# Performance work log

Hardware: AMD Instinct MI355X
Metric: run time of the kernel (lower is better)

Reference implementation:

```python
import jax, jax.numpy as jnp
import numpy as np

N, E, B = 65536, 262144, 2048   # nodes, edges, graphs
ND, ED, H, L = 32, 8, 128, 4    # node feat, edge feat, hidden, egnn layers
PE, PH, CH = 1280, 512, 512     # protein embed, protein hidden, combined hidden
EPS = 1e-8


def _seg_mean(data, ids, num):
    s = jax.ops.segment_sum(data, ids, num_segments=num)
    c = jax.ops.segment_sum(jnp.ones((data.shape[0], 1), data.dtype), ids, num_segments=num)
    return s / jnp.clip(c, 1.0)


def setup_inputs() -> dict:
    key = jax.random.key(0)
    ks = iter(jax.random.split(key, 40))

    def p(shape, scale=0.05):
        return jax.random.normal(next(ks), shape, dtype=jnp.float32) * scale

    inp = {
        "x": jax.random.normal(next(ks), (N, ND), dtype=jnp.float32),
        "pos": jax.random.normal(next(ks), (N, 3), dtype=jnp.float32),
        "edge_attr": jax.random.uniform(next(ks), (E, ED), dtype=jnp.float32),
        "protein_embedding": jax.random.normal(next(ks), (B, PE), dtype=jnp.float32),
        "edge_index": jax.random.randint(next(ks), (2, E), 0, N),
        "batch": jnp.arange(N, dtype=jnp.int64) // (N // B),
        # EGNN embeddings
        "emb_in_w": p((ND, H)), "emb_in_b": p((H,)),
        "emb_out_w": p((H, H)), "emb_out_b": p((H,)),
        # per-layer stacked params (leading dim L)
        "edge_w1": p((L, 2 * H + 1 + ED, H)), "edge_b1": p((L, H)),
        "edge_w2": p((L, H, H)), "edge_b2": p((L, H)),
        "att_w": p((L, H, 1)), "att_b": p((L, 1)),
        "coord_w1": p((L, H, H)), "coord_b1": p((L, H)),
        "coord_w2": p((L, H, 1)),  # no bias, xavier in torch impl
        "node_w1": p((L, 2 * H, H)), "node_b1": p((L, H)),
        "node_w2": p((L, H, H)), "node_b2": p((L, H)),
        # protein + combined heads
        "prot_w": p((PE, PH)), "prot_b": p((PH,)),
        "comb_w1": p((H + PH, CH)), "comb_b1": p((CH,)),
        "comb_w2": p((CH, 1)), "comb_b2": p((1,)),
    }
    return inp


def _forward(x, pos, edge_attr, protein_embedding,
             emb_in_w, emb_in_b, emb_out_w, emb_out_b,
             edge_w1, edge_b1, edge_w2, edge_b2, att_w, att_b,
             coord_w1, coord_b1, coord_w2,
             node_w1, node_b1, node_w2, node_b2,
             prot_w, prot_b, comb_w1, comb_b1, comb_w2, comb_b2,
             edge_index, batch):
    row, col = edge_index[0], edge_index[1]
    h = x @ emb_in_w + emb_in_b
    for l in range(L):
        # coord2radial (normalize=True)
        d = pos[row] - pos[col]                       # [E,3]
        radial = jnp.sum(d * d, axis=-1, keepdims=True)  # [E,1]
        d = d / (jnp.sqrt(radial) + EPS)
        # edge model with sigmoid attention gate
        e_in = jnp.concatenate([h[row], h[col], radial, edge_attr], axis=-1)
        m = jax.nn.silu(e_in @ edge_w1[l] + edge_b1[l])
        m = jax.nn.silu(m @ edge_w2[l] + edge_b2[l])
        m = m * jax.nn.sigmoid(m @ att_w[l] + att_b[l])
        # coord model (tanh=True, coords_agg='mean')
        t = jax.nn.silu(m @ coord_w1[l] + coord_b1[l])
        trans = d * jnp.tanh(t @ coord_w2[l])         # [E,3]
        pos = pos + _seg_mean(trans, row, N)
        # node model (sum aggregation, residual)
        agg = jax.ops.segment_sum(m, row, num_segments=N)
        nh = jax.nn.silu(jnp.concatenate([h, agg], axis=-1) @ node_w1[l] + node_b1[l])
        h = h + (nh @ node_w2[l] + node_b2[l])
    h = h @ emb_out_w + emb_out_b
    # global mean pool over graphs
    drug = _seg_mean(h, batch, B)                     # [B,H]
    prot = jax.nn.relu(protein_embedding @ prot_w + prot_b)  # dropout = identity (eval)
    c = jnp.concatenate([drug, prot], axis=-1)
    c = jax.nn.relu(c @ comb_w1 + comb_b1)
    logits = (c @ comb_w2 + comb_b2)[:, 0]
    return logits


def reference(x, pos, edge_attr, protein_embedding,
              emb_in_w, emb_in_b, emb_out_w, emb_out_b,
              edge_w1, edge_b1, edge_w2, edge_b2, att_w, att_b,
              coord_w1, coord_b1, coord_w2,
              node_w1, node_b1, node_w2, node_b2,
              prot_w, prot_b, comb_w1, comb_b1, comb_w2, comb_b2,
              edge_index, batch):
    logits = _forward(x, pos, edge_attr, protein_embedding,
                      emb_in_w, emb_in_b, emb_out_w, emb_out_b,
                      edge_w1, edge_b1, edge_w2, edge_b2, att_w, att_b,
                      coord_w1, coord_b1, coord_w2,
                      node_w1, node_b1, node_w2, node_b2,
                      prot_w, prot_b, comb_w1, comb_b1, comb_w2, comb_b2,
                      edge_index, batch)
    attention_weights = jnp.zeros((B, 1, 1), dtype=logits.dtype)
    return logits, attention_weights
```

## Files before the change

### kernel.cpp

```cpp
#include <hip/hip_runtime.h>
#include <math.h>


static constexpr int NN  = 65536;
static constexpr int NE  = 262144;
static constexpr int NB  = 2048;
static constexpr int NDF = 32;
static constexpr int HD  = 128;
static constexpr int NL  = 4;
static constexpr int PED = 1280;
static constexpr int PHD = 512;
static constexpr int CHD = 512;
static constexpr float EPSV = 1e-8f;

static constexpr int KK1 = 9;
static constexpr int KK2 = 4;
static constexpr int KKN1 = 8;
static constexpr int KKP = 40;
static constexpr int KKC = 20;

static constexpr int ES = 36;

typedef __attribute__((ext_vector_type(8))) short bf8_t;
typedef __attribute__((ext_vector_type(4))) float f4_t;

__device__ __forceinline__ float sigmoid_f(float x) {
  return __fdividef(1.0f, 1.0f + __expf(-x));
}
__device__ __forceinline__ float silu_f(float x) { return x * sigmoid_f(x); }

__device__ __forceinline__ ushort f2bf(float f) {
  unsigned u = __float_as_uint(f);
  u += 0x7FFFu + ((u >> 16) & 1u);
  return (ushort)(u >> 16);
}
__device__ __forceinline__ float bf2f(ushort h) {
  return __uint_as_float(((unsigned)h) << 16);
}

__device__ __forceinline__ void fma44(float (&acc)[4][4], const float4 a, const float4 w) {
  const float av[4] = {a.x, a.y, a.z, a.w};
  const float wv[4] = {w.x, w.y, w.z, w.w};
#pragma unroll
  for (int i = 0; i < 4; ++i)
#pragma unroll
    for (int j = 0; j < 4; ++j) acc[i][j] = fmaf(av[i], wv[j], acc[i][j]);
}


__global__ void hist_kernel(const int* __restrict__ ei, int* __restrict__ deg) {
  const int e = blockIdx.x * 256 + threadIdx.x;
  if (e < NE) atomicAdd(&deg[ei[e]], 1);
}
// ... 24 lines not shown
    }
    __syncthreads();
    row_ptr[i + 1] = wsums[wave] + incl;
    __syncthreads();
  }
}

__global__ void fill_kernel(const int* __restrict__ ei, const int* __restrict__ row_ptr,
                            int* __restrict__ fill_pos, int* __restrict__ edge_ids) {
  const int e = blockIdx.x * 256 + threadIdx.x;
  if (e < NE) {
    const int n = ei[e];
    const int s = atomicAdd(&fill_pos[n], 1);
    edge_ids[row_ptr[n] + s] = e;
  }
}

__global__ void pos_copy_kernel(const float* __restrict__ pos, float* __restrict__ pc) {
  const int n = blockIdx.x * 256 + threadIdx.x;
  if (n < NN) {
    const float4 v = make_float4(pos[(size_t)n * 3 + 0], pos[(size_t)n * 3 + 1],
                                 pos[(size_t)n * 3 + 2], 0.0f);
    *(float4*)(pc + (size_t)n * 4) = v;
  }
}


__global__ __launch_bounds__(256) void packw_kernel(
    const float* __restrict__ W, ushort* __restrict__ Wp,
    int K, int N, int KK, size_t sW, size_t sWp) {
// ... 13 lines not shown
  for (int p = 0; p < 4; ++p) {
    const int ka = k0 + p * 2, kb = ka + 1;
    const unsigned lo = (ka < K) ? f2bf(w[(size_t)ka * N + n]) : 0;
    const unsigned hi = (kb < K) ? f2bf(w[(size_t)kb * N + n]) : 0;
    ww[p] = lo | (hi << 16);
  }
  *(uint4*)(Wp + layer * sWp + (size_t)i * 8) = make_uint4(ww[0], ww[1], ww[2], ww[3]);
}

__global__ __launch_bounds__(256) void cvt_bf_kernel(const float* __restrict__ in,
                                                     ushort* __restrict__ out, int n) {
  const int i = blockIdx.x * 256 + threadIdx.x;
  if (i * 8 >= n) return;
  const float4 v0 = *(const float4*)(in + (size_t)i * 8);
  const float4 v1 = *(const float4*)(in + (size_t)i * 8 + 4);
  unsigned w0 = (unsigned)f2bf(v0.x) | ((unsigned)f2bf(v0.y) << 16);
  unsigned w1 = (unsigned)f2bf(v0.z) | ((unsigned)f2bf(v0.w) << 16);
  unsigned w2 = (unsigned)f2bf(v1.x) | ((unsigned)f2bf(v1.y) << 16);
  unsigned w3 = (unsigned)f2bf(v1.z) | ((unsigned)f2bf(v1.w) << 16);
  *(uint4*)(out + (size_t)i * 8) = make_uint4(w0, w1, w2, w3);
}


__global__ __launch_bounds__(256) void geom_kernel(
    const float* __restrict__ pos_cur, const float* __restrict__ edge_attr,
    const int* __restrict__ ei, float* __restrict__ dnb, ushort* __restrict__ extra) {
  const int e = blockIdx.x * 256 + threadIdx.x;
  if (e >= NE) return;
  const int r = ei[e], c = ei[NE + e];
  const float4 pr = *(const float4*)(pos_cur + (size_t)r * 4);
  const float4 pc = *(const float4*)(pos_cur + (size_t)c * 4);
  const float dx = pr.x - pc.x, dy = pr.y - pc.y, dz = pr.z - pc.z;
  const float radial = dx * dx + dy * dy + dz * dz;
  const float inv = 1.0f / (sqrtf(radial) + EPSV);
  *(float4*)(dnb + (size_t)e * 4) = make_float4(dx * inv, dy * inv, dz * inv, 0.0f);
  const float4 ea0 = *(const float4*)(edge_attr + (size_t)e * 8);
  const float4 ea1 = *(const float4*)(edge_attr + (size_t)e * 8 + 4);
  const unsigned w0 = (unsigned)f2bf(radial) | ((unsigned)f2bf(ea0.x) << 16);
  const unsigned w1 = (unsigned)f2bf(ea0.y) | ((unsigned)f2bf(ea0.z) << 16);
  const unsigned w2 = (unsigned)f2bf(ea0.w) | ((unsigned)f2bf(ea1.x) << 16);
  const unsigned w3 = (unsigned)f2bf(ea1.y) | ((unsigned)f2bf(ea1.z) << 16);
  const unsigned w4 = (unsigned)f2bf(ea1.w);
  ushort* dst = extra + (size_t)e * 32;
  *(uint4*)(dst)      = make_uint4(w0, w1, w2, w3);
  *(uint4*)(dst + 8)  = make_uint4(w4, 0, 0, 0);
  *(uint4*)(dst + 16) = make_uint4(0, 0, 0, 0);
  *(uint4*)(dst + 24) = make_uint4(0, 0, 0, 0);
}


__global__ __launch_bounds__(256) void emb_in_kernel(
    const float* __restrict__ x, const float* __restrict__ W,
    const float* __restrict__ B, float* __restrict__ h, ushort* __restrict__ hbf) {
  __shared__ float xs[NDF * ES];
  const int t = threadIdx.x;
  const int n0 = blockIdx.x * 32;
  {
    const int r = t >> 3;
    const int kq = (t & 7) * 4;
    const float4 v = *(const float4*)(x + (size_t)(n0 + r) * NDF + kq);
// ... 7 lines not shown
  float acc[4][4] = {};
  const float* wp = W + fg * 4;
#pragma unroll
  for (int k = 0; k < NDF; ++k) {
    const float4 a = *(const float4*)&xs[k * ES + eg * 4];
    const float4 w = *(const float4*)(wp + (size_t)k * HD);
    fma44(acc, a, w);
  }
  const float4 bv = *(const float4*)(B + fg * 4);
  const float bb[4] = {bv.x, bv.y, bv.z, bv.w};
#pragma unroll
  for (int i = 0; i < 4; ++i) {
    const float4 o = make_float4(acc[i][0] + bb[0], acc[i][1] + bb[1],
                                 acc[i][2] + bb[2], acc[i][3] + bb[3]);
    *(float4*)(h + (size_t)(n0 + eg * 4 + i) * HD + fg * 4) = o;
    ushort4 hb;
    hb.x = f2bf(o.x); hb.y = f2bf(o.y); hb.z = f2bf(o.z); hb.w = f2bf(o.w);
    *(ushort4*)(hbf + (size_t)(n0 + eg * 4 + i) * HD + fg * 4) = hb;
  }
}


__global__ __launch_bounds__(256) void edge_mfma_kernel(
    const ushort* __restrict__ hbf, const ushort* __restrict__ extra,
    const int* __restrict__ edge_index, const float* __restrict__ dnb,
    const ushort* __restrict__ W1p, const float* __restrict__ B1,
    const ushort* __restrict__ W2p, const float* __restrict__ B2,
    const float* __restrict__ AW, const float* __restrict__ AB,
    const ushort* __restrict__ CW1p, const float* __restrict__ CB1,
    const float* __restrict__ CW2,
    ushort* __restrict__ m_bf, float* __restrict__ trans_out) {
  __shared__ ushort mtile[64 * 128];
  __shared__ int ridx[64], cidx[64];
  __shared__ float redbuf[2][64];
  __shared__ float gates[64];

  const int t = threadIdx.x;
  const int e0 = blockIdx.x * 64;
  if (t < 64) {
    ridx[t] = edge_index[e0 + t];
    cidx[t] = edge_index[NE + e0 + t];
  }
  __syncthreads();

  const int w = t >> 6, l = t & 63;
  const int wr = w >> 1, wc = w & 1;
  const int g = l >> 4, ln = l & 15;
  const int row0 = wr * 32;

  int er[2], ec[2], rowA[2];
#pragma unroll
  for (int mt = 0; mt < 2; ++mt) {
    rowA[mt] = row0 + mt * 16 + ln;
    er[mt] = ridx[rowA[mt]];
    ec[mt] = cidx[rowA[mt]];
  }

  const f4_t zf = {0.0f, 0.0f, 0.0f, 0.0f};
  f4_t acc[2][4];
#pragma unroll
  for (int mt = 0; mt < 2; ++mt)
#pragma unroll
    for (int nt = 0; nt < 4; ++nt) acc[mt][nt] = zf;

#pragma unroll
  for (int kk = 0; kk < KK1; ++kk) {
    bf8_t a[2], b[4];
#pragma unroll
    for (int mt = 0; mt < 2; ++mt) {
      if (kk < 8) {
        const int idx = (kk < 4) ? er[mt] : ec[mt];
        a[mt] = *(const bf8_t*)(hbf + (size_t)idx * HD + (kk & 3) * 32 + g * 8);
      } else {
        a[mt] = *(const bf8_t*)(extra + (size_t)(e0 + rowA[mt]) * 32 + g * 8);
      }
    }
#pragma unroll
    for (int nt = 0; nt < 4; ++nt)
      b[nt] = *(const bf8_t*)(W1p + ((size_t)(kk * 8 + wc * 4 + nt) * 64 + l) * 8);
#pragma unroll
    for (int mt = 0; mt < 2; ++mt)
#pragma unroll
      for (int nt = 0; nt < 4; ++nt)
        acc[mt][nt] = __builtin_amdgcn_mfma_f32_16x16x32_bf16(a[mt], b[nt], acc[mt][nt], 0, 0, 0);
  }

  {
    float bn[4];
#pragma unroll
    for (int nt = 0; nt < 4; ++nt) bn[nt] = B1[wc * 64 + nt * 16 + ln];
#pragma unroll
    for (int mt = 0; mt < 2; ++mt)
#pragma unroll
      for (int nt = 0; nt < 4; ++nt) {
        const int col = wc * 64 + nt * 16 + ln;
#pragma unroll
        for (int r = 0; r < 4; ++r) {
          const int row = row0 + mt * 16 + g * 4 + r;
          const float v = silu_f(acc[mt][nt][r] + bn[nt]);
          mtile[row * HD + (col ^ ((row & 7) << 3))] = f2bf(v);
        }
      }
  }
  __syncthreads();

  f4_t acc2[2][4];
#pragma unroll
  for (int mt = 0; mt < 2; ++mt)
#pragma unroll
    for (int nt = 0; nt < 4; ++nt) acc2[mt][nt] = zf;
#pragma unroll
  for (int kk = 0; kk < KK2; ++kk) {
    bf8_t a[2], b[4];
#pragma unroll
    for (int mt = 0; mt < 2; ++mt) {
      const int ra = rowA[mt];
      const int k0 = kk * 32 + g * 8;
      a[mt] = *(const bf8_t*)&mtile[ra * HD + (k0 ^ ((ra & 7) << 3))];
    }
#pragma unroll
    for (int nt = 0; nt < 4; ++nt)
      b[nt] = *(const bf8_t*)(W2p + ((size_t)(kk * 8 + wc * 4 + nt) * 64 + l) * 8);
#pragma unroll
    for (int mt = 0; mt < 2; ++mt)
#pragma unroll
      for (int nt = 0; nt < 4; ++nt)
        acc2[mt][nt] = __builtin_amdgcn_mfma_f32_16x16x32_bf16(a[mt], b[nt], acc2[mt][nt], 0, 0, 0);
  }

  float m2v[2][4][4];
  {
    float bn[4], awv[4];
#pragma unroll
    for (int nt = 0; nt < 4; ++nt) {
      const int col = wc * 64 + nt * 16 + ln;
      bn[nt] = B2[col];
      awv[nt] = AW[col];
    }
    float p[2][4] = {{0, 0, 0, 0}, {0, 0, 0, 0}};
#pragma unroll
    for (int mt = 0; mt < 2; ++mt)
#pragma unroll
      for (int nt = 0; nt < 4; ++nt)
#pragma unroll
        for (int r = 0; r < 4; ++r) {
          const float v = silu_f(acc2[mt][nt][r] + bn[nt]);
          m2v[mt][nt][r] = v;
          p[mt][r] = fmaf(v, awv[nt], p[mt][r]);
        }
#pragma unroll
    for (int mt = 0; mt < 2; ++mt)
#pragma unroll
      for (int r = 0; r < 4; ++r) {
#pragma unroll
        for (int d = 1; d < 16; d <<= 1) p[mt][r] += __shfl_xor(p[mt][r], d, 64);
      }
    if (ln == 0) {
#pragma unroll
      for (int mt = 0; mt < 2; ++mt)
#pragma unroll
        for (int r = 0; r < 4; ++r)
          redbuf[wc][row0 + mt * 16 + g * 4 + r] = p[mt][r];
    }
  }
  __syncthreads();
  if (t < 64) gates[t] = sigmoid_f(redbuf[0][t] + redbuf[1][t] + AB[0]);
  __syncthreads();

  {
    float grow[2][4];
#pragma unroll
    for (int mt = 0; mt < 2; ++mt)
#pragma unroll
      for (int r = 0; r < 4; ++r) grow[mt][r] = gates[row0 + mt * 16 + g * 4 + r];
#pragma unroll
    for (int mt = 0; mt < 2; ++mt)
#pragma unroll
      for (int nt = 0; nt < 4; ++nt) {
        const int col = wc * 64 + nt * 16 + ln;
#pragma unroll
        for (int r = 0; r < 4; ++r) {
          const int row = row0 + mt * 16 + g * 4 + r;
          mtile[row * HD + (col ^ ((row & 7) << 3))] = f2bf(m2v[mt][nt][r] * grow[mt][r]);
        }
      }
  }
  __syncthreads();

  f4_t acc3[2][4];
#pragma unroll
  for (int mt = 0; mt < 2; ++mt)
#pragma unroll
    for (int nt = 0; nt < 4; ++nt) acc3[mt][nt] = zf;
#pragma unroll
  for (int kk = 0; kk < KK2; ++kk) {
    bf8_t a[2], b[4];
#pragma unroll
    for (int mt = 0; mt < 2; ++mt) {
      const int ra = rowA[mt];
      const int k0 = kk * 32 + g * 8;
      a[mt] = *(const bf8_t*)&mtile[ra * HD + (k0 ^ ((ra & 7) << 3))];
    }
#pragma unroll
    for (int nt = 0; nt < 4; ++nt)
      b[nt] = *(const bf8_t*)(CW1p + ((size_t)(kk * 8 + wc * 4 + nt) * 64 + l) * 8);
#pragma unroll
    for (int mt = 0; mt < 2; ++mt)
#pragma unroll
      for (int nt = 0; nt < 4; ++nt)
        acc3[mt][nt] = __builtin_amdgcn_mfma_f32_16x16x32_bf16(a[mt], b[nt], acc3[mt][nt], 0, 0, 0);
  }
  {
    float cb[4], cwv[4];
#pragma unroll
    for (int nt = 0; nt < 4; ++nt) {
      const int col = wc * 64 + nt * 16 + ln;
      cb[nt] = CB1[col];
      cwv[nt] = CW2[col];
    }
    float q[2][4] = {{0, 0, 0, 0}, {0, 0, 0, 0}};
#pragma unroll
    for (int mt = 0; mt < 2; ++mt)
#pragma unroll
      for (int nt = 0; nt < 4; ++nt)
#pragma unroll
        for (int r = 0; r < 4; ++r) {
          const float v = silu_f(acc3[mt][nt][r] + cb[nt]);
          q[mt][r] = fmaf(v, cwv[nt], q[mt][r]);
        }
#pragma unroll
    for (int mt = 0; mt < 2; ++mt)
#pragma unroll
      for (int r = 0; r < 4; ++r) {
#pragma unroll
        for (int d = 1; d < 16; d <<= 1) q[mt][r] += __shfl_xor(q[mt][r], d, 64);
      }
    if (ln == 0) {
#pragma unroll
      for (int mt = 0; mt < 2; ++mt)
#pragma unroll
        for (int r = 0; r < 4; ++r)
          redbuf[wc][row0 + mt * 16 + g * 4 + r] = q[mt][r];
    }
  }
  __syncthreads();
  if (t < 64) {
    const float s = tanhf(redbuf[0][t] + redbuf[1][t]);
    const f4_t dn = *(const f4_t*)(dnb + (size_t)(e0 + t) * 4);
    const f4_t tr = dn * s;
    *(f4_t*)(trans_out + (size_t)(e0 + t) * 4) = tr;
  }

#pragma unroll
  for (int it = 0; it < 4; ++it) {
    const int i = it * 256 + t;
    const int row = i >> 4;
    const int c8 = (i & 15) * 8;
    const uint4 v = *(const uint4*)&mtile[row * HD + (c8 ^ ((row & 7) << 3))];
    *(uint4*)(m_bf + (size_t)(e0 + row) * HD + c8) = v;
  }
}


__global__ __launch_bounds__(256) void gather_kernel(
    const ushort* __restrict__ m_bf, const float* __restrict__ trans,
    const int* __restrict__ row_ptr, const int* __restrict__ edge_ids,
    ushort* __restrict__ agg_bf, float* __restrict__ pos_cur) {
  const int t = threadIdx.x;
  const int wave = t >> 6, lane = t & 63;
  const int n = blockIdx.x * 4 + wave;
  const int s = row_ptr[n], e_end = row_ptr[n + 1];
  float a0 = 0.0f, a1 = 0.0f, ta = 0.0f;
  for (int i = s; i < e_end; ++i) {
    const int e = edge_ids[i];
    const ushort2 v = *(const ushort2*)(m_bf + (size_t)e * HD + lane * 2);
    a0 += bf2f(v.x);
    a1 += bf2f(v.y);
    if (lane < 4) ta += trans[(size_t)e * 4 + lane];
  }
  ushort2 ab;
  ab.x = f2bf(a0);
  ab.y = f2bf(a1);
  *(ushort2*)(agg_bf + (size_t)n * HD + lane * 2) = ab;
  if (lane < 3) {
    const int dg = e_end - s;
    pos_cur[(size_t)n * 4 + lane] += ta / (float)(dg > 0 ? dg : 1);
  }
}


__global__ __launch_bounds__(256) void node_mfma_kernel(
    float* __restrict__ h, const ushort* __restrict__ hbf,
    const ushort* __restrict__ agg_bf,
    const ushort* __restrict__ W1p, const float* __restrict__ B1,
    const ushort* __restrict__ W2p, const float* __restrict__ B2,
    ushort* __restrict__ hbf_out) {
  __shared__ ushort mtile[64 * 128];
  const int t = threadIdx.x;
  const int n0 = blockIdx.x * 64;
  const int w = t >> 6, l = t & 63;
  const int wr = w >> 1, wc = w & 1;
  const int g = l >> 4, ln = l & 15;
  const int row0 = wr * 32;
  int rowA[2];
#pragma unroll
  for (int mt = 0; mt < 2; ++mt) rowA[mt] = row0 + mt * 16 + ln;

  const f4_t zf = {0.0f, 0.0f, 0.0f, 0.0f};
  f4_t acc[2][4];
#pragma unroll
  for (int mt = 0; mt < 2; ++mt)
#pragma unroll
    for (int nt = 0; nt < 4; ++nt) acc[mt][nt] = zf;

#pragma unroll
  for (int kk = 0; kk < KKN1; ++kk) {
    bf8_t a[2], b[4];
#pragma unroll
    for (int mt = 0; mt < 2; ++mt) {
      const size_t base = (size_t)(n0 + rowA[mt]) * HD + (kk & 3) * 32 + g * 8;
      a[mt] = (kk < 4) ? *(const bf8_t*)(hbf + base) : *(const bf8_t*)(agg_bf + base);
    }
#pragma unroll
    for (int nt = 0; nt < 4; ++nt)
      b[nt] = *(const bf8_t*)(W1p + ((size_t)(kk * 8 + wc * 4 + nt) * 64 + l) * 8);
#pragma unroll
    for (int mt = 0; mt < 2; ++mt)
#pragma unroll
      for (int nt = 0; nt < 4; ++nt)
        acc[mt][nt] = __builtin_amdgcn_mfma_f32_16x16x32_bf16(a[mt], b[nt], acc[mt][nt], 0, 0, 0);
  }
  {
    float bn[4];
#pragma unroll
    for (int nt = 0; nt < 4; ++nt) bn[nt] = B1[wc * 64 + nt * 16 + ln];
#pragma unroll
    for (int mt = 0; mt < 2; ++mt)
#pragma unroll
      for (int nt = 0; nt < 4; ++nt) {
        const int col = wc * 64 + nt * 16 + ln;
#pragma unroll
        for (int r = 0; r < 4; ++r) {
          const int row = row0 + mt * 16 + g * 4 + r;
          const float v = silu_f(acc[mt][nt][r] + bn[nt]);
          mtile[row * HD + (col ^ ((row & 7) << 3))] = f2bf(v);
        }
      }
  }
  __syncthreads();

  f4_t acc2[2][4];
#pragma unroll
  for (int mt = 0; mt < 2; ++mt)
#pragma unroll
    for (int nt = 0; nt < 4; ++nt) acc2[mt][nt] = zf;
#pragma unroll
  for (int kk = 0; kk < KK2; ++kk) {
    bf8_t a[2], b[4];
#pragma unroll
    for (int mt = 0; mt < 2; ++mt) {
      const int ra = rowA[mt];
      const int k0 = kk * 32 + g * 8;
      a[mt] = *(const bf8_t*)&mtile[ra * HD + (k0 ^ ((ra & 7) << 3))];
    }
#pragma unroll
    for (int nt = 0; nt < 4; ++nt)
      b[nt] = *(const bf8_t*)(W2p + ((size_t)(kk * 8 + wc * 4 + nt) * 64 + l) * 8);
#pragma unroll
    for (int mt = 0; mt < 2; ++mt)
#pragma unroll
      for (int nt = 0; nt < 4; ++nt)
        acc2[mt][nt] = __builtin_amdgcn_mfma_f32_16x16x32_bf16(a[mt], b[nt], acc2[mt][nt], 0, 0, 0);
  }
  {
    float bn[4];
#pragma unroll
    for (int nt = 0; nt < 4; ++nt) bn[nt] = B2[wc * 64 + nt * 16 + ln];
#pragma unroll
    for (int mt = 0; mt < 2; ++mt)
#pragma unroll
      for (int nt = 0; nt < 4; ++nt) {
        const int col = wc * 64 + nt * 16 + ln;
#pragma unroll
        for (int r = 0; r < 4; ++r) {
          const int row = row0 + mt * 16 + g * 4 + r;
          float* hp = h + (size_t)(n0 + row) * HD + col;
          const float o = *hp + acc2[mt][nt][r] + bn[nt];
          *hp = o;
          hbf_out[(size_t)(n0 + row) * HD + col] = f2bf(o);
        }
      }
  }
}


__global__ __launch_bounds__(256) void gemm_head_kernel(
    const ushort* __restrict__ A, const ushort* __restrict__ Wp,
    const float* __restrict__ bias, ushort* __restrict__ out,
    int lda, int KK, int NTG, int ldo, int col_off) {
  const int t = threadIdx.x;
  const int rb = blockIdx.x * 64;
  const int cb = blockIdx.y * 128;
  const int w = t >> 6, l = t & 63;
  const int wr = w >> 1, wc = w & 1;
  const int g = l >> 4, ln = l & 15;
  const int row0 = wr * 32;
// ... 115 lines not shown

  char* ws = (char*)d_ws;
  size_t off = 0;
  auto carve = [&](size_t bytes) -> void* {
    void* p = ws + off;
    off += (bytes + 255) & ~(size_t)255;
    return p;
  };
  float*  h       = (float*)carve((size_t)NN * HD * 4);
  ushort* h_bf    = (ushort*)carve((size_t)NN * HD * 2);
  ushort* agg_bf  = (ushort*)carve((size_t)NN * HD * 2);
  ushort* m_bf    = (ushort*)carve((size_t)NE * HD * 2);
  float*  trans   = (float*)carve((size_t)NE * 4 * 4);
  float*  dnb     = (float*)carve((size_t)NE * 4 * 4);
  ushort* extra   = (ushort*)carve((size_t)NE * 32 * 2);
  float*  pos_cur = (float*)carve((size_t)NN * 4 * 4);
  ushort* pe_bf   = (ushort*)carve((size_t)NB * PED * 2);
  ushort* c_in    = (ushort*)carve((size_t)NB * (HD + PHD) * 2);
  ushort* c1      = (ushort*)carve((size_t)NB * CHD * 2);
  const size_t sW1p  = (size_t)KK1 * 8 * 64 * 8;
  const size_t sW2p  = (size_t)KK2 * 8 * 64 * 8;
  const size_t sNW1p = (size_t)KKN1 * 8 * 64 * 8;
  const size_t sPWp  = (size_t)KKP * 32 * 64 * 8;
  const size_t sCWp  = (size_t)KKC * 32 * 64 * 8;
  ushort* W1p     = (ushort*)carve(sW1p * NL * 2);
  ushort* W2p     = (ushort*)carve(sW2p * NL * 2);
  ushort* CW1p    = (ushort*)carve(sW2p * NL * 2);
  ushort* NW1p    = (ushort*)carve(sNW1p * NL * 2);
  ushort* NW2p    = (ushort*)carve(sW2p * NL * 2);
  ushort* PWp     = (ushort*)carve(sPWp * 2);
  ushort* CWp     = (ushort*)carve(sCWp * 2);
  int* deg        = (int*)carve((size_t)NN * 4);
  int* row_ptr    = (int*)carve((size_t)(NN + 1) * 4);
  int* fill_pos   = (int*)carve((size_t)NN * 4);
  int* edge_ids   = (int*)carve((size_t)NE * 4);

  hipMemsetAsync(deg, 0, (size_t)NN * 4, stream);
  hipMemsetAsync(fill_pos, 0, (size_t)NN * 4, stream);

  pos_copy_kernel<<<NN / 256, 256, 0, stream>>>(pos, pos_cur);
  hist_kernel<<<NE / 256, 256, 0, stream>>>(edge_index, deg);
  scan_kernel<<<1, 1024, 0, stream>>>(deg, row_ptr);
  fill_kernel<<<NE / 256, 256, 0, stream>>>(edge_index, row_ptr, fill_pos, edge_ids);

  packw_kernel<<<dim3(18, NL), 256, 0, stream>>>(edge_w1, W1p, 265, HD, KK1,
                                                 (size_t)265 * HD, sW1p);
  packw_kernel<<<dim3(8, NL), 256, 0, stream>>>(edge_w2, W2p, HD, HD, KK2,
                                                (size_t)HD * HD, sW2p);
  packw_kernel<<<dim3(8, NL), 256, 0, stream>>>(coord_w1, CW1p, HD, HD, KK2,
                                                (size_t)HD * HD, sW2p);
  packw_kernel<<<dim3(16, NL), 256, 0, stream>>>(node_w1, NW1p, 2 * HD, HD, KKN1,
                                                 (size_t)2 * HD * HD, sNW1p);
  packw_kernel<<<dim3(8, NL), 256, 0, stream>>>(node_w2, NW2p, HD, HD, KK2,
                                                (size_t)HD * HD, sW2p);
  packw_kernel<<<dim3(320, 1), 256, 0, stream>>>(prot_w, PWp, PED, PHD, KKP, 0, 0);
  packw_kernel<<<dim3(160, 1), 256, 0, stream>>>(comb_w1, CWp, HD + PHD, CHD, KKC, 0, 0);

  cvt_bf_kernel<<<NB * PED / (256 * 8), 256, 0, stream>>>(pe, pe_bf, NB * PED);

  emb_in_kernel<<<NN / 32, 256, 0, stream>>>(x, emb_in_w, emb_in_b, h, h_bf);

  for (int l = 0; l < NL; ++l) {
    geom_kernel<<<NE / 256, 256, 0, stream>>>(pos_cur, edge_attr, edge_index,
                                              dnb, extra);
    edge_mfma_kernel<<<NE / 64, 256, 0, stream>>>(
        h_bf, extra, edge_index, dnb,
        W1p + (size_t)l * sW1p, edge_b1 + (size_t)l * HD,
        W2p + (size_t)l * sW2p, edge_b2 + (size_t)l * HD,
        att_w + (size_t)l * HD, att_b + l,
        CW1p + (size_t)l * sW2p, coord_b1 + (size_t)l * HD,
        coord_w2 + (size_t)l * HD,
        m_bf, trans);
    gather_kernel<<<NN / 4, 256, 0, stream>>>(m_bf, trans, row_ptr, edge_ids,
                                              agg_bf, pos_cur);
    node_mfma_kernel<<<NN / 64, 256, 0, stream>>>(
        h, h_bf, agg_bf,
        NW1p + (size_t)l * sNW1p, node_b1 + (size_t)l * HD,
        NW2p + (size_t)l * sW2p, node_b2 + (size_t)l * HD, h_bf);
  }

  pool_kernel<<<NB, 128, 0, stream>>>(h, emb_out_w, emb_out_b, c_in);
  gemm_head_kernel<<<dim3(NB / 64, PHD / 128), 256, 0, stream>>>(
      pe_bf, PWp, prot_b, c_in, PED, KKP, PHD / 16, HD + PHD, HD);
  gemm_head_kernel<<<dim3(NB / 64, CHD / 128), 256, 0, stream>>>(
      c_in, CWp, comb_b1, c1, HD + PHD, KKC, CHD / 16, CHD, 0);
  logits_kernel<<<NB / 4, 256, 0, stream>>>(c1, comb_w2, comb_b2, out);
}
```

Measured before the change: 1.094 ms.

## Sort edges by destination and transpose MFMA operand roles in edge/node kernels

Edges are permuted once into CSR order (row/col and edge_attr copied into sorted buffers), so the per-layer geometry and edge kernels produce messages already grouped by source node. The gather kernel can then read messages contiguously instead of going through an edge_ids indirection. The edge and node MFMA kernels also swap operand roles: weights become the A operand and edges or nodes the B operand. This gives each lane four contiguous output features, which allows vectorised bias loads, packed bf16 stores and shorter shuffle reductions. The cost is a one-time permutation pass plus extra buffers for the sorted indices and attributes.

```diff
diff --git a/kernel.cpp b/kernel.cpp
--- a/kernel.cpp
+++ b/kernel.cpp
@@ -37,6 +37,9 @@
 __device__ __forceinline__ float bf2f(ushort h) {
   return __uint_as_float(((unsigned)h) << 16);
 }
+__device__ __forceinline__ unsigned pk2bf(float a, float b) {
+  return (unsigned)f2bf(a) | ((unsigned)f2bf(b) << 16);
+}
 
 __device__ __forceinline__ void fma44(float (&acc)[4][4], const float4 a, const float4 w) {
   const float av[4] = {a.x, a.y, a.z, a.w};
@@ -91,6 +94,21 @@
     const int s = atomicAdd(&fill_pos[n], 1);
     edge_ids[row_ptr[n] + s] = e;
   }
+}
+
+__global__ void perm_kernel(const int* __restrict__ ei, const int* __restrict__ edge_ids,
+                            const float* __restrict__ edge_attr,
+                            int* __restrict__ rowp, int* __restrict__ colp,
+                            float* __restrict__ eap) {
+  const int i = blockIdx.x * 256 + threadIdx.x;
+  if (i >= NE) return;
+  const int e = edge_ids[i];
+  rowp[i] = ei[e];
+  colp[i] = ei[NE + e];
+  const float4 a = *(const float4*)(edge_attr + (size_t)e * 8);
+  const float4 b = *(const float4*)(edge_attr + (size_t)e * 8 + 4);
+  *(float4*)(eap + (size_t)i * 8) = a;
+  *(float4*)(eap + (size_t)i * 8 + 4) = b;
 }
 
 __global__ void pos_copy_kernel(const float* __restrict__ pos, float* __restrict__ pc) {
@@ -134,36 +152,30 @@
   if (i * 8 >= n) return;
   const float4 v0 = *(const float4*)(in + (size_t)i * 8);
   const float4 v1 = *(const float4*)(in + (size_t)i * 8 + 4);
-  unsigned w0 = (unsigned)f2bf(v0.x) | ((unsigned)f2bf(v0.y) << 16);
-  unsigned w1 = (unsigned)f2bf(v0.z) | ((unsigned)f2bf(v0.w) << 16);
-  unsigned w2 = (unsigned)f2bf(v1.x) | ((unsigned)f2bf(v1.y) << 16);
-  unsigned w3 = (unsigned)f2bf(v1.z) | ((unsigned)f2bf(v1.w) << 16);
-  *(uint4*)(out + (size_t)i * 8) = make_uint4(w0, w1, w2, w3);
+  *(uint4*)(out + (size_t)i * 8) =
+      make_uint4(pk2bf(v0.x, v0.y), pk2bf(v0.z, v0.w), pk2bf(v1.x, v1.y), pk2bf(v1.z, v1.w));
 }
 
 
 __global__ __launch_bounds__(256) void geom_kernel(
-    const float* __restrict__ pos_cur, const float* __restrict__ edge_attr,
-    const int* __restrict__ ei, float* __restrict__ dnb, ushort* __restrict__ extra) {
-  const int e = blockIdx.x * 256 + threadIdx.x;
-  if (e >= NE) return;
-  const int r = ei[e], c = ei[NE + e];
+    const float* __restrict__ pos_cur, const float* __restrict__ eap,
+    const int* __restrict__ rowp, const int* __restrict__ colp,
+    float* __restrict__ dnb, ushort* __restrict__ extra) {
+  const int i = blockIdx.x * 256 + threadIdx.x;
+  if (i >= NE) return;
+  const int r = rowp[i], c = colp[i];
   const float4 pr = *(const float4*)(pos_cur + (size_t)r * 4);
   const float4 pc = *(const float4*)(pos_cur + (size_t)c * 4);
   const float dx = pr.x - pc.x, dy = pr.y - pc.y, dz = pr.z - pc.z;
   const float radial = dx * dx + dy * dy + dz * dz;
   const float inv = 1.0f / (sqrtf(radial) + EPSV);
-  *(float4*)(dnb + (size_t)e * 4) = make_float4(dx * inv, dy * inv, dz * inv, 0.0f);
-  const float4 ea0 = *(const float4*)(edge_attr + (size_t)e * 8);
-  const float4 ea1 = *(const float4*)(edge_attr + (size_t)e * 8 + 4);
-  const unsigned w0 = (unsigned)f2bf(radial) | ((unsigned)f2bf(ea0.x) << 16);
-  const unsigned w1 = (unsigned)f2bf(ea0.y) | ((unsigned)f2bf(ea0.z) << 16);
-  const unsigned w2 = (unsigned)f2bf(ea0.w) | ((unsigned)f2bf(ea1.x) << 16);
-  const unsigned w3 = (unsigned)f2bf(ea1.y) | ((unsigned)f2bf(ea1.z) << 16);
-  const unsigned w4 = (unsigned)f2bf(ea1.w);
-  ushort* dst = extra + (size_t)e * 32;
-  *(uint4*)(dst)      = make_uint4(w0, w1, w2, w3);
-  *(uint4*)(dst + 8)  = make_uint4(w4, 0, 0, 0);
+  *(float4*)(dnb + (size_t)i * 4) = make_float4(dx * inv, dy * inv, dz * inv, 0.0f);
+  const float4 ea0 = *(const float4*)(eap + (size_t)i * 8);
+  const float4 ea1 = *(const float4*)(eap + (size_t)i * 8 + 4);
+  ushort* dst = extra + (size_t)i * 32;
+  *(uint4*)(dst) = make_uint4(pk2bf(radial, ea0.x), pk2bf(ea0.y, ea0.z),
+                              pk2bf(ea0.w, ea1.x), pk2bf(ea1.y, ea1.z));
+  *(uint4*)(dst + 8)  = make_uint4((unsigned)f2bf(ea1.w), 0, 0, 0);
   *(uint4*)(dst + 16) = make_uint4(0, 0, 0, 0);
   *(uint4*)(dst + 24) = make_uint4(0, 0, 0, 0);
 }
@@ -201,23 +213,23 @@
     const float4 o = make_float4(acc[i][0] + bb[0], acc[i][1] + bb[1],
                                  acc[i][2] + bb[2], acc[i][3] + bb[3]);
     *(float4*)(h + (size_t)(n0 + eg * 4 + i) * HD + fg * 4) = o;
-    ushort4 hb;
-    hb.x = f2bf(o.x); hb.y = f2bf(o.y); hb.z = f2bf(o.z); hb.w = f2bf(o.w);
-    *(ushort4*)(hbf + (size_t)(n0 + eg * 4 + i) * HD + fg * 4) = hb;
+    *(uint2*)(hbf + (size_t)(n0 + eg * 4 + i) * HD + fg * 4) =
+        make_uint2(pk2bf(o.x, o.y), pk2bf(o.z, o.w));
   }
 }
 
 
 __global__ __launch_bounds__(256) void edge_mfma_kernel(
     const ushort* __restrict__ hbf, const ushort* __restrict__ extra,
-    const int* __restrict__ edge_index, const float* __restrict__ dnb,
+    const int* __restrict__ rowp, const int* __restrict__ colp,
+    const float* __restrict__ dnb,
     const ushort* __restrict__ W1p, const float* __restrict__ B1,
     const ushort* __restrict__ W2p, const float* __restrict__ B2,
     const float* __restrict__ AW, const float* __restrict__ AB,
     const ushort* __restrict__ CW1p, const float* __restrict__ CB1,
     const float* __restrict__ CW2,
     ushort* __restrict__ m_bf, float* __restrict__ trans_out) {
-  __shared__ ushort mtile[64 * 128];
+  __shared__ ushort mtileT[64 * 128];
   __shared__ int ridx[64], cidx[64];
   __shared__ float redbuf[2][64];
   __shared__ float gates[64];
@@ -225,209 +237,186 @@
   const int t = threadIdx.x;
   const int e0 = blockIdx.x * 64;
   if (t < 64) {
-    ridx[t] = edge_index[e0 + t];
-    cidx[t] = edge_index[NE + e0 + t];
+    ridx[t] = rowp[e0 + t];
+    cidx[t] = colp[e0 + t];
   }
   __syncthreads();
 
   const int w = t >> 6, l = t & 63;
-  const int wr = w >> 1, wc = w & 1;
+  const int wn = w & 1, we = w >> 1;
   const int g = l >> 4, ln = l & 15;
-  const int row0 = wr * 32;
-
-  int er[2], ec[2], rowA[2];
-#pragma unroll
-  for (int mt = 0; mt < 2; ++mt) {
-    rowA[mt] = row0 + mt * 16 + ln;
-    er[mt] = ridx[rowA[mt]];
-    ec[mt] = cidx[rowA[mt]];
+  const int nb = wn * 64;
+  const int eb = we * 32;
+
+  int je[2], er[2], ec[2], swz[2];
+#pragma unroll
+  for (int et = 0; et < 2; ++et) {
+    je[et] = eb + et * 16 + ln;
+    er[et] = ridx[je[et]];
+    ec[et] = cidx[je[et]];
+    swz[et] = (je[et] & 7) << 3;
   }
 
   const f4_t zf = {0.0f, 0.0f, 0.0f, 0.0f};
-  f4_t acc[2][4];
-#pragma unroll
-  for (int mt = 0; mt < 2; ++mt)
-#pragma unroll
-    for (int nt = 0; nt < 4; ++nt) acc[mt][nt] = zf;
+  f4_t acc[4][2];
+#pragma unroll
+  for (int mt = 0; mt < 4; ++mt)
+#pragma unroll
+    for (int et = 0; et < 2; ++et) acc[mt][et] = zf;
 
 #pragma unroll
   for (int kk = 0; kk < KK1; ++kk) {
-    bf8_t a[2], b[4];
-#pragma unroll
-    for (int mt = 0; mt < 2; ++mt) {
+    bf8_t aw[4], be[2];
+#pragma unroll
+    for (int mt = 0; mt < 4; ++mt)
+      aw[mt] = *(const bf8_t*)(W1p + ((size_t)(kk * 8 + wn * 4 + mt) * 64 + l) * 8);
+#pragma unroll
+    for (int et = 0; et < 2; ++et) {
       if (kk < 8) {
-        const int idx = (kk < 4) ? er[mt] : ec[mt];
-        a[mt] = *(const bf8_t*)(hbf + (size_t)idx * HD + (kk & 3) * 32 + g * 8);
+        const int idx = (kk < 4) ? er[et] : ec[et];
+        be[et] = *(const bf8_t*)(hbf + (size_t)idx * HD + (kk & 3) * 32 + g * 8);
       } else {
-        a[mt] = *(const bf8_t*)(extra + (size_t)(e0 + rowA[mt]) * 32 + g * 8);
+        be[et] = *(const bf8_t*)(extra + (size_t)(e0 + je[et]) * 32 + g * 8);
       }
     }
 #pragma unroll
-    for (int nt = 0; nt < 4; ++nt)
-      b[nt] = *(const bf8_t*)(W1p + ((size_t)(kk * 8 + wc * 4 + nt) * 64 + l) * 8);
-#pragma unroll
-    for (int mt = 0; mt < 2; ++mt)
-#pragma unroll
-      for (int nt = 0; nt < 4; ++nt)
-        acc[mt][nt] = __builtin_amdgcn_mfma_f32_16x16x32_bf16(a[mt], b[nt], acc[mt][nt], 0, 0, 0);
+    for (int mt = 0; mt < 4; ++mt)
+#pragma unroll
+      for (int et = 0; et < 2; ++et)
+        acc[mt][et] = __builtin_amdgcn_mfma_f32_16x16x32_bf16(aw[mt], be[et], acc[mt][et], 0, 0, 0);
   }
 
   {
-    float bn[4];
-#pragma unroll
-    for (int nt = 0; nt < 4; ++nt) bn[nt] = B1[wc * 64 + nt * 16 + ln];
-#pragma unroll
-    for (int mt = 0; mt < 2; ++mt)
-#pragma unroll
-      for (int nt = 0; nt < 4; ++nt) {
-        const int col = wc * 64 + nt * 16 + ln;
+#pragma unroll
+    for (int mt = 0; mt < 4; ++mt) {
+      const int n0 = nb + mt * 16 + g * 4;
+      const float4 bv = *(const float4*)(B1 + n0);
+#pragma unroll
+      for (int et = 0; et < 2; ++et) {
+        const unsigned lo = pk2bf(silu_f(acc[mt][et][0] + bv.x), silu_f(acc[mt][et][1] + bv.y));
+        const unsigned hi = pk2bf(silu_f(acc[mt][et][2] + bv.z), silu_f(acc[mt][et][3] + bv.w));
+        *(uint2*)&mtileT[je[et] * HD + (n0 ^ swz[et])] = make_uint2(lo, hi);
+      }
+    }
+  }
+  __syncthreads();
+
+  f4_t acc2[4][2];
+#pragma unroll
+  for (int mt = 0; mt < 4; ++mt)
+#pragma unroll
+    for (int et = 0; et < 2; ++et) acc2[mt][et] = zf;
+#pragma unroll
+  for (int kk = 0; kk < KK2; ++kk) {
+    bf8_t aw[4], be[2];
+#pragma unroll
+    for (int mt = 0; mt < 4; ++mt)
+      aw[mt] = *(const bf8_t*)(W2p + ((size_t)(kk * 8 + wn * 4 + mt) * 64 + l) * 8);
+    const int nk = kk * 32 + g * 8;
+#pragma unroll
+    for (int et = 0; et < 2; ++et)
+      be[et] = *(const bf8_t*)&mtileT[je[et] * HD + (nk ^ swz[et])];
+#pragma unroll
+    for (int mt = 0; mt < 4; ++mt)
+#pragma unroll
+      for (int et = 0; et < 2; ++et)
+        acc2[mt][et] = __builtin_amdgcn_mfma_f32_16x16x32_bf16(aw[mt], be[et], acc2[mt][et], 0, 0, 0);
+  }
+
+  float m2v[4][2][4];
+  {
+    float p[2] = {0.0f, 0.0f};
+#pragma unroll
+    for (int mt = 0; mt < 4; ++mt) {
+      const int n0 = nb + mt * 16 + g * 4;
+      const float4 bv = *(const float4*)(B2 + n0);
+      const float4 av = *(const float4*)(AW + n0);
+      const float bb[4] = {bv.x, bv.y, bv.z, bv.w};
+      const float aa[4] = {av.x, av.y, av.z, av.w};
+#pragma unroll
+      for (int et = 0; et < 2; ++et)
 #pragma unroll
         for (int r = 0; r < 4; ++r) {
-          const int row = row0 + mt * 16 + g * 4 + r;
-          const float v = silu_f(acc[mt][nt][r] + bn[nt]);
-          mtile[row * HD + (col ^ ((row & 7) << 3))] = f2bf(v);
+          const float v = silu_f(acc2[mt][et][r] + bb[r]);
+          m2v[mt][et][r] = v;
+          p[et] = fmaf(v, aa[r], p[et]);
         }
+    }
+#pragma unroll
+    for (int et = 0; et < 2; ++et) {
+      p[et] += __shfl_xor(p[et], 16, 64);
+      p[et] += __shfl_xor(p[et], 32, 64);
+    }
+    if (l < 16) {
+#pragma unroll
+      for (int et = 0; et < 2; ++et) redbuf[wn][eb + et * 16 + l] = p[et];
+    }
+  }
+  __syncthreads();
+  if (t < 64) gates[t] = sigmoid_f(redbuf[0][t] + redbuf[1][t] + AB[0]);
+  __syncthreads();
+
+  {
+    float grow[2];
+#pragma unroll
+    for (int et = 0; et < 2; ++et) grow[et] = gates[je[et]];
+#pragma unroll
+    for (int mt = 0; mt < 4; ++mt) {
+      const int n0 = nb + mt * 16 + g * 4;
+#pragma unroll
+      for (int et = 0; et < 2; ++et) {
+        const unsigned lo = pk2bf(m2v[mt][et][0] * grow[et], m2v[mt][et][1] * grow[et]);
+        const unsigned hi = pk2bf(m2v[mt][et][2] * grow[et], m2v[mt][et][3] * grow[et]);
+        *(uint2*)&mtileT[je[et] * HD + (n0 ^ swz[et])] = make_uint2(lo, hi);
       }
-  }
-  __syncthreads();
-
-  f4_t acc2[2][4];
-#pragma unroll
-  for (int mt = 0; mt < 2; ++mt)
-#pragma unroll
-    for (int nt = 0; nt < 4; ++nt) acc2[mt][nt] = zf;
+    }
+  }
+  __syncthreads();
+
+  f4_t acc3[4][2];
+#pragma unroll
+  for (int mt = 0; mt < 4; ++mt)
+#pragma unroll
+    for (int et = 0; et < 2; ++et) acc3[mt][et] = zf;
 #pragma unroll
   for (int kk = 0; kk < KK2; ++kk) {
-    bf8_t a[2], b[4];
-#pragma unroll
-    for (int mt = 0; mt < 2; ++mt) {
-      const int ra = rowA[mt];
-      const int k0 = kk * 32 + g * 8;
-      a[mt] = *(const bf8_t*)&mtile[ra * HD + (k0 ^ ((ra & 7) << 3))];
-    }
-#pragma unroll
-    for (int nt = 0; nt < 4; ++nt)
-      b[nt] = *(const bf8_t*)(W2p + ((size_t)(kk * 8 + wc * 4 + nt) * 64 + l) * 8);
-#pragma unroll
-    for (int mt = 0; mt < 2; ++mt)
-#pragma unroll
-      for (int nt = 0; nt < 4; ++nt)
-        acc2[mt][nt] = __builtin_amdgcn_mfma_f32_16x16x32_bf16(a[mt], b[nt], acc2[mt][nt], 0, 0, 0);
-  }
-
-  float m2v[2][4][4];
+    bf8_t aw[4], be[2];
+#pragma unroll
+    for (int mt = 0; mt < 4; ++mt)
+      aw[mt] = *(const bf8_t*)(CW1p + ((size_t)(kk * 8 + wn * 4 + mt) * 64 + l) * 8);
+    const int nk = kk * 32 + g * 8;
+#pragma unroll
+    for (int et = 0; et < 2; ++et)
+      be[et] = *(const bf8_t*)&mtileT[je[et] * HD + (nk ^ swz[et])];
+#pragma unroll
+    for (int mt = 0; mt < 4; ++mt)
+#pragma unroll
+      for (int et = 0; et < 2; ++et)
+        acc3[mt][et] = __builtin_amdgcn_mfma_f32_16x16x32_bf16(aw[mt], be[et], acc3[mt][et], 0, 0, 0);
+  }
   {
-    float bn[4], awv[4];
-#pragma unroll
-    for (int nt = 0; nt < 4; ++nt) {
-      const int col = wc * 64 + nt * 16 + ln;
-      bn[nt] = B2[col];
-      awv[nt] = AW[col];
-    }
-    float p[2][4] = {{0, 0, 0, 0}, {0, 0, 0, 0}};
-#pragma unroll
-    for (int mt = 0; mt < 2; ++mt)
-#pragma unroll
-      for (int nt = 0; nt < 4; ++nt)
-#pragma unroll
-        for (int r = 0; r < 4; ++r) {
-          const float v = silu_f(acc2[mt][nt][r] + bn[nt]);
-          m2v[mt][nt][r] = v;
-          p[mt][r] = fmaf(v, awv[nt], p[mt][r]);
-        }
-#pragma unroll
-    for (int mt = 0; mt < 2; ++mt)
-#pragma unroll
-      for (int r = 0; r < 4; ++r) {
-#pragma unroll
-        for (int d = 1; d < 16; d <<= 1) p[mt][r] += __shfl_xor(p[mt][r], d, 64);
-      }
-    if (ln == 0) {
-#pragma unroll
-      for (int mt = 0; mt < 2; ++mt)
+    float q[2] = {0.0f, 0.0f};
+#pragma unroll
+    for (int mt = 0; mt < 4; ++mt) {
+      const int n0 = nb + mt * 16 + g * 4;
+      const float4 bv = *(const float4*)(CB1 + n0);
+      const float4 cv = *(const float4*)(CW2 + n0);
+      const float bb[4] = {bv.x, bv.y, bv.z, bv.w};
+      const float cc[4] = {cv.x, cv.y, cv.z, cv.w};
+#pragma unroll
+      for (int et = 0; et < 2; ++et)
 #pragma unroll
         for (int r = 0; r < 4; ++r)
-          redbuf[wc][row0 + mt * 16 + g * 4 + r] = p[mt][r];
-    }
-  }
-  __syncthreads();
-  if (t < 64) gates[t] = sigmoid_f(redbuf[0][t] + redbuf[1][t] + AB[0]);
-  __syncthreads();
-
-  {
-    float grow[2][4];
-#pragma unroll
-    for (int mt = 0; mt < 2; ++mt)
-#pragma unroll
-      for (int r = 0; r < 4; ++r) grow[mt][r] = gates[row0 + mt * 16 + g * 4 + r];
-#pragma unroll
-    for (int mt = 0; mt < 2; ++mt)
-#pragma unroll
-      for (int nt = 0; nt < 4; ++nt) {
-        const int col = wc * 64 + nt * 16 + ln;
-#pragma unroll
-        for (int r = 0; r < 4; ++r) {
-          const int row = row0 + mt * 16 + g * 4 + r;
-          mtile[row * HD + (col ^ ((row & 7) << 3))] = f2bf(m2v[mt][nt][r] * grow[mt][r]);
-        }
-      }
-  }
-  __syncthreads();
-
-  f4_t acc3[2][4];
-#pragma unroll
-  for (int mt = 0; mt < 2; ++mt)
-#pragma unroll
-    for (int nt = 0; nt < 4; ++nt) acc3[mt][nt] = zf;
-#pragma unroll
-  for (int kk = 0; kk < KK2; ++kk) {
-    bf8_t a[2], b[4];
-#pragma unroll
-    for (int mt = 0; mt < 2; ++mt) {
-      const int ra = rowA[mt];
-      const int k0 = kk * 32 + g * 8;
-      a[mt] = *(const bf8_t*)&mtile[ra * HD + (k0 ^ ((ra & 7) << 3))];
-    }
-#pragma unroll
-    for (int nt = 0; nt < 4; ++nt)
-      b[nt] = *(const bf8_t*)(CW1p + ((size_t)(kk * 8 + wc * 4 + nt) * 64 + l) * 8);
-#pragma unroll
-    for (int mt = 0; mt < 2; ++mt)
-#pragma unroll
-      for (int nt = 0; nt < 4; ++nt)
-        acc3[mt][nt] = __builtin_amdgcn_mfma_f32_16x16x32_bf16(a[mt], b[nt], acc3[mt][nt], 0, 0, 0);
-  }
-  {
-    float cb[4], cwv[4];
-#pragma unroll
-    for (int nt = 0; nt < 4; ++nt) {
-      const int col = wc * 64 + nt * 16 + ln;
-      cb[nt] = CB1[col];
-      cwv[nt] = CW2[col];
-    }
-    float q[2][4] = {{0, 0, 0, 0}, {0, 0, 0, 0}};
-#pragma unroll
-    for (int mt = 0; mt < 2; ++mt)
-#pragma unroll
-      for (int nt = 0; nt < 4; ++nt)
-#pragma unroll
-        for (int r = 0; r < 4; ++r) {
-          const float v = silu_f(acc3[mt][nt][r] + cb[nt]);
-          q[mt][r] = fmaf(v, cwv[nt], q[mt][r]);
-        }
-#pragma unroll
-    for (int mt = 0; mt < 2; ++mt)
-#pragma unroll
-      for (int r = 0; r < 4; ++r) {
-#pragma unroll
-        for (int d = 1; d < 16; d <<= 1) q[mt][r] += __shfl_xor(q[mt][r], d, 64);
-      }
-    if (ln == 0) {
-#pragma unroll
-      for (int mt = 0; mt < 2; ++mt)
-#pragma unroll
-        for (int r = 0; r < 4; ++r)
-          redbuf[wc][row0 + mt * 16 + g * 4 + r] = q[mt][r];
+          q[et] = fmaf(silu_f(acc3[mt][et][r] + bb[r]), cc[r], q[et]);
+    }
+#pragma unroll
+    for (int et = 0; et < 2; ++et) {
+      q[et] += __shfl_xor(q[et], 16, 64);
+      q[et] += __shfl_xor(q[et], 32, 64);
+    }
+    if (l < 16) {
+#pragma unroll
+      for (int et = 0; et < 2; ++et) redbuf[wn][eb + et * 16 + l] = q[et];
     }
   }
   __syncthreads();
@@ -443,7 +432,7 @@
     const int i = it * 256 + t;
     const int row = i >> 4;
     const int c8 = (i & 15) * 8;
-    const uint4 v = *(const uint4*)&mtile[row * HD + (c8 ^ ((row & 7) << 3))];
+    const uint4 v = *(const uint4*)&mtileT[row * HD + (c8 ^ ((row & 7) << 3))];
     *(uint4*)(m_bf + (size_t)(e0 + row) * HD + c8) = v;
   }
 }
@@ -451,7 +440,7 @@
 
 __global__ __launch_bounds__(256) void gather_kernel(
     const ushort* __restrict__ m_bf, const float* __restrict__ trans,
-    const int* __restrict__ row_ptr, const int* __restrict__ edge_ids,
+    const int* __restrict__ row_ptr,
     ushort* __restrict__ agg_bf, float* __restrict__ pos_cur) {
   const int t = threadIdx.x;
   const int wave = t >> 6, lane = t & 63;
@@ -459,11 +448,10 @@
   const int s = row_ptr[n], e_end = row_ptr[n + 1];
   float a0 = 0.0f, a1 = 0.0f, ta = 0.0f;
   for (int i = s; i < e_end; ++i) {
-    const int e = edge_ids[i];
-    const ushort2 v = *(const ushort2*)(m_bf + (size_t)e * HD + lane * 2);
+    const ushort2 v = *(const ushort2*)(m_bf + (size_t)i * HD + lane * 2);
     a0 += bf2f(v.x);
     a1 += bf2f(v.y);
-    if (lane < 4) ta += trans[(size_t)e * 4 + lane];
+    if (lane < 4) ta += trans[(size_t)i * 4 + lane];
   }
   ushort2 ab;
   ab.x = f2bf(a0);
@@ -482,101 +470,101 @@
     const ushort* __restrict__ W1p, const float* __restrict__ B1,
     const ushort* __restrict__ W2p, const float* __restrict__ B2,
     ushort* __restrict__ hbf_out) {
-  __shared__ ushort mtile[64 * 128];
+  __shared__ ushort mtileT[64 * 128];
   const int t = threadIdx.x;
-  const int n0 = blockIdx.x * 64;
+  const int n0blk = blockIdx.x * 64;
   const int w = t >> 6, l = t & 63;
-  const int wr = w >> 1, wc = w & 1;
+  const int wn = w & 1, we = w >> 1;
   const int g = l >> 4, ln = l & 15;
-  const int row0 = wr * 32;
-  int rowA[2];
-#pragma unroll
-  for (int mt = 0; mt < 2; ++mt) rowA[mt] = row0 + mt * 16 + ln;
+  const int nb = wn * 64;
+  const int eb = we * 32;
+
+  int jn[2], swz[2];
+#pragma unroll
+  for (int et = 0; et < 2; ++et) {
+    jn[et] = eb + et * 16 + ln;
+    swz[et] = (jn[et] & 7) << 3;
+  }
 
   const f4_t zf = {0.0f, 0.0f, 0.0f, 0.0f};
-  f4_t acc[2][4];
-#pragma unroll
-  for (int mt = 0; mt < 2; ++mt)
-#pragma unroll
-    for (int nt = 0; nt < 4; ++nt) acc[mt][nt] = zf;
+  f4_t acc[4][2];
+#pragma unroll
+  for (int mt = 0; mt < 4; ++mt)
+#pragma unroll
+    for (int et = 0; et < 2; ++et) acc[mt][et] = zf;
 
 #pragma unroll
   for (int kk = 0; kk < KKN1; ++kk) {
-    bf8_t a[2], b[4];
-#pragma unroll
-    for (int mt = 0; mt < 2; ++mt) {
-      const size_t base = (size_t)(n0 + rowA[mt]) * HD + (kk & 3) * 32 + g * 8;
-      a[mt] = (kk < 4) ? *(const bf8_t*)(hbf + base) : *(const bf8_t*)(agg_bf + base);
-    }
-#pragma unroll
-    for (int nt = 0; nt < 4; ++nt)
-      b[nt] = *(const bf8_t*)(W1p + ((size_t)(kk * 8 + wc * 4 + nt) * 64 + l) * 8);
-#pragma unroll
-    for (int mt = 0; mt < 2; ++mt)
-#pragma unroll
-      for (int nt = 0; nt < 4; ++nt)
-        acc[mt][nt] = __builtin_amdgcn_mfma_f32_16x16x32_bf16(a[mt], b[nt], acc[mt][nt], 0, 0, 0);
+    bf8_t aw[4], be[2];
+#pragma unroll
+    for (int mt = 0; mt < 4; ++mt)
+      aw[mt] = *(const bf8_t*)(W1p + ((size_t)(kk * 8 + wn * 4 + mt) * 64 + l) * 8);
+#pragma unroll
+    for (int et = 0; et < 2; ++et) {
+      const size_t base = (size_t)(n0blk + jn[et]) * HD + (kk & 3) * 32 + g * 8;
+      be[et] = (kk < 4) ? *(const bf8_t*)(hbf + base) : *(const bf8_t*)(agg_bf + base);
+    }
+#pragma unroll
+    for (int mt = 0; mt < 4; ++mt)
+#pragma unroll
+      for (int et = 0; et < 2; ++et)
+        acc[mt][et] = __builtin_amdgcn_mfma_f32_16x16x32_bf16(aw[mt], be[et], acc[mt][et], 0, 0, 0);
   }
   {
-    float bn[4];
-#pragma unroll
-    for (int nt = 0; nt < 4; ++nt) bn[nt] = B1[wc * 64 + nt * 16 + ln];
-#pragma unroll
-    for (int mt = 0; mt < 2; ++mt)
-#pragma unroll
-      for (int nt = 0; nt < 4; ++nt) {
-        const int col = wc * 64 + nt * 16 + ln;
-#pragma unroll
-        for (int r = 0; r < 4; ++r) {
-          const int row = row0 + mt * 16 + g * 4 + r;
-          const float v = silu_f(acc[mt][nt][r] + bn[nt]);
-          mtile[row * HD + (col ^ ((row & 7) << 3))] = f2bf(v);
-        }
+#pragma unroll
+    for (int mt = 0; mt < 4; ++mt) {
+      const int n0 = nb + mt * 16 + g * 4;
+      const float4 bv = *(const float4*)(B1 + n0);
+#pragma unroll
+      for (int et = 0; et < 2; ++et) {
+        const unsigned lo = pk2bf(silu_f(acc[mt][et][0] + bv.x), silu_f(acc[mt][et][1] + bv.y));
+        const unsigned hi = pk2bf(silu_f(acc[mt][et][2] + bv.z), silu_f(acc[mt][et][3] + bv.w));
+        *(uint2*)&mtileT[jn[et] * HD + (n0 ^ swz[et])] = make_uint2(lo, hi);
       }
-  }
-  __syncthreads();
-
-  f4_t acc2[2][4];
-#pragma unroll
-  for (int mt = 0; mt < 2; ++mt)
-#pragma unroll
-    for (int nt = 0; nt < 4; ++nt) acc2[mt][nt] = zf;
+    }
+  }
+  __syncthreads();
+
+  f4_t acc2[4][2];
+#pragma unroll
+  for (int mt = 0; mt < 4; ++mt)
+#pragma unroll
+    for (int et = 0; et < 2; ++et) acc2[mt][et] = zf;
 #pragma unroll
   for (int kk = 0; kk < KK2; ++kk) {
-    bf8_t a[2], b[4];
-#pragma unroll
-    for (int mt = 0; mt < 2; ++mt) {
-      const int ra = rowA[mt];
-      const int k0 = kk * 32 + g * 8;
-      a[mt] = *(const bf8_t*)&mtile[ra * HD + (k0 ^ ((ra & 7) << 3))];
-    }
-#pragma unroll
-    for (int nt = 0; nt < 4; ++nt)
-      b[nt] = *(const bf8_t*)(W2p + ((size_t)(kk * 8 + wc * 4 + nt) * 64 + l) * 8);
-#pragma unroll
-    for (int mt = 0; mt < 2; ++mt)
-#pragma unroll
-      for (int nt = 0; nt < 4; ++nt)
-        acc2[mt][nt] = __builtin_amdgcn_mfma_f32_16x16x32_bf16(a[mt], b[nt], acc2[mt][nt], 0, 0, 0);
+    bf8_t aw[4], be[2];
+#pragma unroll
+    for (int mt = 0; mt < 4; ++mt)
+      aw[mt] = *(const bf8_t*)(W2p + ((size_t)(kk * 8 + wn * 4 + mt) * 64 + l) * 8);
+    const int nk = kk * 32 + g * 8;
+#pragma unroll
+    for (int et = 0; et < 2; ++et)
+      be[et] = *(const bf8_t*)&mtileT[jn[et] * HD + (nk ^ swz[et])];
+#pragma unroll
+    for (int mt = 0; mt < 4; ++mt)
+#pragma unroll
+      for (int et = 0; et < 2; ++et)
+        acc2[mt][et] = __builtin_amdgcn_mfma_f32_16x16x32_bf16(aw[mt], be[et], acc2[mt][et], 0, 0, 0);
   }
   {
-    float bn[4];
-#pragma unroll
-    for (int nt = 0; nt < 4; ++nt) bn[nt] = B2[wc * 64 + nt * 16 + ln];
-#pragma unroll
-    for (int mt = 0; mt < 2; ++mt)
-#pragma unroll
-      for (int nt = 0; nt < 4; ++nt) {
-        const int col = wc * 64 + nt * 16 + ln;
-#pragma unroll
-        for (int r = 0; r < 4; ++r) {
-          const int row = row0 + mt * 16 + g * 4 + r;
-          float* hp = h + (size_t)(n0 + row) * HD + col;
-          const float o = *hp + acc2[mt][nt][r] + bn[nt];
-          *hp = o;
-          hbf_out[(size_t)(n0 + row) * HD + col] = f2bf(o);
-        }
+#pragma unroll
+    for (int mt = 0; mt < 4; ++mt) {
+      const int n0 = nb + mt * 16 + g * 4;
+      const float4 bv = *(const float4*)(B2 + n0);
+#pragma unroll
+      for (int et = 0; et < 2; ++et) {
+        float* hp = h + (size_t)(n0blk + jn[et]) * HD + n0;
+        const float4 old = *(const float4*)hp;
+        float4 o;
+        o.x = old.x + acc2[mt][et][0] + bv.x;
+        o.y = old.y + acc2[mt][et][1] + bv.y;
+        o.z = old.z + acc2[mt][et][2] + bv.z;
+        o.w = old.w + acc2[mt][et][3] + bv.w;
+        *(float4*)hp = o;
+        *(uint2*)(hbf_out + (size_t)(n0blk + jn[et]) * HD + n0) =
+            make_uint2(pk2bf(o.x, o.y), pk2bf(o.z, o.w));
       }
+    }
   }
 }
 
@@ -722,6 +710,7 @@
   float*  trans   = (float*)carve((size_t)NE * 4 * 4);
   float*  dnb     = (float*)carve((size_t)NE * 4 * 4);
   ushort* extra   = (ushort*)carve((size_t)NE * 32 * 2);
+  float*  eap     = (float*)carve((size_t)NE * 8 * 4);
   float*  pos_cur = (float*)carve((size_t)NN * 4 * 4);
   ushort* pe_bf   = (ushort*)carve((size_t)NB * PED * 2);
   ushort* c_in    = (ushort*)carve((size_t)NB * (HD + PHD) * 2);
@@ -742,6 +731,8 @@
   int* row_ptr    = (int*)carve((size_t)(NN + 1) * 4);
   int* fill_pos   = (int*)carve((size_t)NN * 4);
   int* edge_ids   = (int*)carve((size_t)NE * 4);
+  int* rowp       = (int*)carve((size_t)NE * 4);
+  int* colp       = (int*)carve((size_t)NE * 4);
 
   hipMemsetAsync(deg, 0, (size_t)NN * 4, stream);
   hipMemsetAsync(fill_pos, 0, (size_t)NN * 4, stream);
@@ -750,6 +741,8 @@
   hist_kernel<<<NE / 256, 256, 0, stream>>>(edge_index, deg);
   scan_kernel<<<1, 1024, 0, stream>>>(deg, row_ptr);
   fill_kernel<<<NE / 256, 256, 0, stream>>>(edge_index, row_ptr, fill_pos, edge_ids);
+  perm_kernel<<<NE / 256, 256, 0, stream>>>(edge_index, edge_ids, edge_attr,
+                                            rowp, colp, eap);
 
   packw_kernel<<<dim3(18, NL), 256, 0, stream>>>(edge_w1, W1p, 265, HD, KK1,
                                                  (size_t)265 * HD, sW1p);
@@ -769,18 +762,16 @@
   emb_in_kernel<<<NN / 32, 256, 0, stream>>>(x, emb_in_w, emb_in_b, h, h_bf);
 
   for (int l = 0; l < NL; ++l) {
-    geom_kernel<<<NE / 256, 256, 0, stream>>>(pos_cur, edge_attr, edge_index,
-                                              dnb, extra);
+    geom_kernel<<<NE / 256, 256, 0, stream>>>(pos_cur, eap, rowp, colp, dnb, extra);
     edge_mfma_kernel<<<NE / 64, 256, 0, stream>>>(
-        h_bf, extra, edge_index, dnb,
+        h_bf, extra, rowp, colp, dnb,
         W1p + (size_t)l * sW1p, edge_b1 + (size_t)l * HD,
         W2p + (size_t)l * sW2p, edge_b2 + (size_t)l * HD,
         att_w + (size_t)l * HD, att_b + l,
         CW1p + (size_t)l * sW2p, coord_b1 + (size_t)l * HD,
         coord_w2 + (size_t)l * HD,
         m_bf, trans);
-    gather_kernel<<<NN / 4, 256, 0, stream>>>(m_bf, trans, row_ptr, edge_ids,
-                                              agg_bf, pos_cur);
+    gather_kernel<<<NN / 4, 256, 0, stream>>>(m_bf, trans, row_ptr, agg_bf, pos_cur);
     node_mfma_kernel<<<NN / 64, 256, 0, stream>>>(
         h, h_bf, agg_bf,
         NW1p + (size_t)l * sNW1p, node_b1 + (size_t)l * HD,
```

Result: faster. 1.026 ms (-6.2%).
